# Kernel optimization log

Measured on AMD Instinct MI355X. Metric: run time of the kernel, lower is better.

## Reference

```python
import jax, jax.numpy as jnp
import numpy as np

# ---- Clifford algebra Cl(3,0): 8 blades ordered by grade: [1, e1,e2,e3, e12,e13,e23, e123] ----
_ORDER = [0, 1, 2, 4, 3, 5, 6, 7]  # bitmask of each blade in grade-sorted order
GRADES = np.array([0, 1, 1, 1, 2, 2, 2, 3])  # grade (subspace) of each blade
EPS = 1e-6

def _build_cayley():
    C = np.zeros((8, 8, 8), np.float32)
    for ia, a in enumerate(_ORDER):
        for ib, b in enumerate(_ORDER):
            # reordering sign from anticommuting basis vectors (Euclidean metric -> squares +1)
            t, tot = a >> 1, 0
            while t:
                tot += bin(t & b).count("1")
                t >>= 1
            s = 1.0 if tot % 2 == 0 else -1.0
            C[ia, ib, _ORDER.index(a ^ b)] = s
    return jnp.asarray(C)

CAYLEY = _build_cayley()  # [8,8,8], highly sparse (64 nonzeros)

def mvlinear(x, W, b):
    # x: [B,N,Cin,8], W: [Cout,Cin,4] per-grade weights, b: [Cout] bias on scalar blade
    Wf = W[:, :, GRADES]                               # [Cout,Cin,8] via repeat over grades [1,3,3,1]
    y = jnp.einsum("bnci,oci->bnoi", x, Wf)
    return y.at[..., 0].add(b)

def setup_inputs() -> dict:
    key = jax.random.key(0)
    ks = jax.random.split(key, 5)
    B, N, Cin, Ch = 8, 4096, 64, 128
    return {
        "x": jax.random.normal(ks[0], (B, N, Cin, 8), jnp.float32),
        "W1": jax.random.normal(ks[1], (Ch, Cin, 4), jnp.float32) / np.sqrt(Cin),
        "b1": jax.random.normal(ks[2], (Ch,), jnp.float32) * 0.02,
        "W2": jax.random.normal(ks[3], (Cin, Ch, 4), jnp.float32) / np.sqrt(Ch),
        "b2": jax.random.normal(ks[4], (Cin,), jnp.float32) * 0.02,
        "a": jnp.ones((Cin,), jnp.float32),
    }

def reference(x, W1, b1, W2, b2, a):
    h = mvlinear(x, W1, b1)                                   # [B,N,Ch,8]
    h = jnp.einsum("bnci,ijk,bncj->bnck", h, CAYLEY, h)       # geometric product (sparse Cayley)
    y = mvlinear(h, W2, b2)                                   # [B,N,Cin,8]
    # MVLayerNorm: per-channel multivector norm (Euclidean: sqrt(sum of squares)),
    # averaged over channels, then scale by learned a
    norm = jnp.sqrt(jnp.sum(y * y, axis=-1, keepdims=True))   # [B,N,Cin,1]
    denom = jnp.mean(norm, axis=-2, keepdims=True) + EPS      # [B,N,1,1]
    return a[None, None, :, None] * y / denom
```

## Files before the change

### kernel.cpp

```cpp
#include <hip/hip_runtime.h>
#include <stdint.h>

typedef unsigned short u16;
typedef __attribute__((ext_vector_type(4))) float f32x4;
typedef __attribute__((ext_vector_type(8))) __bf16 bf16x8;

struct Cay { int idx[8][8]; float sgn[8][8]; };
constexpr int kOrder[8] = {0,1,2,4,3,5,6,7};
constexpr int ordpos(int m){ int r=-1; for(int i=0;i<8;i++) if(kOrder[i]==m) r=i; return r; }
constexpr Cay make_cay(){
  Cay c{};
  for(int ia=0; ia<8; ia++) for(int ib=0; ib<8; ib++){
    int a=kOrder[ia], b=kOrder[ib];
    int t=a>>1, tot=0;
    while(t){ int x=t&b; while(x){ tot+=x&1; x>>=1; } t>>=1; }
    c.idx[ia][ib]=ordpos(a^b);
    c.sgn[ia][ib]=(tot&1)?-1.0f:1.0f;
  }
  return c;
}
constexpr Cay CAY = make_cay();

struct GPTab { float dsgn[8]; int np; int pi[28]; int pj[28]; int pk[28]; float ps[28]; };
constexpr GPTab make_gptab(){
  GPTab t{};
  for (int i=0;i<8;i++) t.dsgn[i] = CAY.sgn[i][i];
  t.np = 0;
  for (int i=0;i<8;i++) for (int j=i+1;j<8;j++){
    float s = CAY.sgn[i][j] + CAY.sgn[j][i];
    if (s != 0.0f){ t.pi[t.np]=i; t.pj[t.np]=j; t.pk[t.np]=CAY.idx[i][j];
                    t.ps[t.np]=(s>0.f)?1.0f:-1.0f; t.np++; }
  }
  return t;
}
constexpr GPTab GPT = make_gptab();

__device__ __forceinline__ void gprod_half(const float* h, float* g){
  float g0 = h[0]*h[0];
  #pragma unroll
  for (int i=1;i<8;i++) g0 = fmaf(GPT.dsgn[i]>0.f ? h[i] : -h[i], h[i], g0);
  g[0] = g0;
  #pragma unroll
  for (int k=1;k<8;k++) g[k] = 0.f;
  #pragma unroll
  for (int t=0;t<GPT.np;t++)
    g[GPT.pk[t]] = fmaf(GPT.ps[t]>0.f ? h[GPT.pi[t]] : -h[GPT.pi[t]],
                        h[GPT.pj[t]], g[GPT.pk[t]]);
}

__device__ __forceinline__ u16 f2bf(float f){
  union { float f; uint32_t u; } v; v.f=f;
  uint32_t u=v.u;
  return (u16)((u + 0x7fffu + ((u>>16)&1u)) >> 16);
}

__device__ __forceinline__ uint32_t cvtpk(float lo, float hi){
  uint32_t r;
  asm("v_cvt_pk_bf16_f32 %0, %1, %2" : "=v"(r) : "v"(lo), "v"(hi));
  return r;
}

__global__ void gp_prepack(const float* __restrict__ W1, const float* __restrict__ W2,
                           u16* __restrict__ w1p, u16* __restrict__ w2p)
{
  int t = blockIdx.x*256 + threadIdx.x;
  int e = t & 7, l = (t>>3)&63, f = t>>9;
  int lm = l & 15, lh = l >> 4;
  if (f < 64) {
    int g = f >> 4, ks = (f>>3)&1, ot = f&7;
    int o = ot*16 + lm, c = ks*32 + lh*8 + e;
    w1p[f*512 + l*8 + e] = f2bf(W1[(o*64 + c)*4 + g]);
  } else {
    int f2 = f - 64;
    int g = f2 >> 4, ks = (f2>>2)&3, ot = f2&3;
    int outc = ot*16 + lm, o = ks*32 + lh*8 + e;
    float sc = (g == 0) ? 1.0f : 2.0f;
    w2p[f2*512 + l*8 + e] = f2bf(W2[(outc*128 + o)*4 + g] * sc);
  }
}

__global__ __launch_bounds__(256,4) void gp_fused(
    const float* __restrict__ x, const u16* __restrict__ w1p,
    const float* __restrict__ b1, const u16* __restrict__ w2p,
    const float* __restrict__ b2, const float* __restrict__ avec,
    float* __restrict__ out)
{
  __shared__ __align__(16) char SH[33024];
  float* redArr = reinterpret_cast<float*>(SH + 32768);
  char* G0 = SH + 16384;

  const int tid = threadIdx.x;
  const int w  = tid >> 6;
  const int l  = tid & 63;
  const int lm = l & 15;
  const int lh = l >> 4;
  const int xk = (lm & 7) << 4;

  constexpr int BSTART[4] = {0,1,4,7};
  constexpr int BCNT[4]   = {1,3,3,1};

  const float4* xb  = reinterpret_cast<const float4*>(x);
  const uint4*  w1f = reinterpret_cast<const uint4*>(w1p);
  const uint4*  w2f = reinterpret_cast<const uint4*>(w2p);
  const float4* b1f = reinterpret_cast<const float4*>(b1);

  const int oc = w*16 + lm;
  const float b2v  = b2[oc];
  const float aval = avec[oc];

  {
    const int cp = tid & 31;
    const int pr = tid >> 5;
    const float4* xt = xb + (size_t)blockIdx.x * 2048;
    #pragma unroll
    for (int it=0; it<2; ++it){
      const int p = pr + it*8;
      const float4* src = xt + p*128 + cp*4;
      float4 v0 = src[0], v1 = src[1], v2 = src[2], v3 = src[3];
      uint32_t pk[8];
      pk[0]=cvtpk(v0.x,v2.x); pk[1]=cvtpk(v0.y,v2.y); pk[2]=cvtpk(v0.z,v2.z); pk[3]=cvtpk(v0.w,v2.w);
      pk[4]=cvtpk(v1.x,v3.x); pk[5]=cvtpk(v1.y,v3.y); pk[6]=cvtpk(v1.z,v3.z); pk[7]=cvtpk(v1.w,v3.w);
      const int xo = (p & 7) << 4;
      #pragma unroll
      for (int b=0;b<8;b++)
        *reinterpret_cast<uint32_t*>(SH + (((p*8+b)<<7) + ((cp<<2) ^ xo))) = pk[b];
    }
  }
  __syncthreads();

  {
    f32x4 acc1[8];
    #pragma unroll
    for (int b=0;b<8;++b) acc1[b] = (f32x4){0.f,0.f,0.f,0.f};
    #pragma unroll
    for (int g4=0; g4<4; ++g4){
      #pragma unroll
      for (int ks=0; ks<2; ++ks){
        uint4 wu = w1f[((g4*2+ks)*8 + w)*64 + l];
        bf16x8 wv = __builtin_bit_cast(bf16x8, wu);
        #pragma unroll
        for (int bi=0; bi<3; ++bi){
          if (bi >= BCNT[g4]) break;
          const int blade = BSTART[g4] + bi;
          bf16x8 xv = *reinterpret_cast<const bf16x8*>(
              SH + (((lm*8+blade)<<7) + (((ks*32+lh*8)<<1) ^ xk)));
          acc1[blade] = __builtin_amdgcn_mfma_f32_16x16x32_bf16(wv, xv, acc1[blade], 0,0,0);
        }
      }
    }
    const float4 b14 = b1f[w*4 + lh];
    const float bb[4] = {b14.x, b14.y, b14.z, b14.w};
    uint32_t glo[8], ghi[8];
    #pragma unroll
    for (int rp=0; rp<2; ++rp){
      float ga[8], gb[8];
      { float h[8];
        #pragma unroll
        for (int b=0;b<8;b++) h[b] = acc1[b][rp*2+0];
        h[0] += bb[rp*2+0]; gprod_half(h, ga); }
      { float h[8];
        #pragma unroll
        for (int b=0;b<8;b++) h[b] = acc1[b][rp*2+1];
        h[0] += bb[rp*2+1]; gprod_half(h, gb); }
      #pragma unroll
      for (int b=0;b<8;b++){
        uint32_t v = cvtpk(ga[b], gb[b]);
        if (rp==0) glo[b] = v; else ghi[b] = v;
      }
    }
    const int chB = w*32 + lh*8;
    #pragma unroll
    for (int b=0;b<8;b++){
      uint2 v; v.x = glo[b]; v.y = ghi[b];
      *reinterpret_cast<uint2*>(G0 + (((lm*8+b)<<7) + (chB ^ xk))) = v;
    }
  }
  __syncthreads();

  uint32_t g1lo[8], g1hi[8];
  {
    f32x4 acc1[8];
    #pragma unroll
    for (int b=0;b<8;++b) acc1[b] = (f32x4){0.f,0.f,0.f,0.f};
    #pragma unroll
    for (int g4=0; g4<4; ++g4){
      #pragma unroll
      for (int ks=0; ks<2; ++ks){
        uint4 wu = w1f[((g4*2+ks)*8 + w + 4)*64 + l];
        bf16x8 wv = __builtin_bit_cast(bf16x8, wu);
        #pragma unroll
        for (int bi=0; bi<3; ++bi){
          if (bi >= BCNT[g4]) break;
          const int blade = BSTART[g4] + bi;
          bf16x8 xv = *reinterpret_cast<const bf16x8*>(
              SH + (((lm*8+blade)<<7) + (((ks*32+lh*8)<<1) ^ xk)));
          acc1[blade] = __builtin_amdgcn_mfma_f32_16x16x32_bf16(wv, xv, acc1[blade], 0,0,0);
        }
      }
    }
    const float4 b14 = b1f[(w+4)*4 + lh];
    const float bb[4] = {b14.x, b14.y, b14.z, b14.w};
    #pragma unroll
    for (int rp=0; rp<2; ++rp){
      float ga[8], gb[8];
      { float h[8];
        #pragma unroll
        for (int b=0;b<8;b++) h[b] = acc1[b][rp*2+0];
        h[0] += bb[rp*2+0]; gprod_half(h, ga); }
      { float h[8];
        #pragma unroll
        for (int b=0;b<8;b++) h[b] = acc1[b][rp*2+1];
        h[0] += bb[rp*2+1]; gprod_half(h, gb); }
      #pragma unroll
      for (int b=0;b<8;b++){
        uint32_t v = cvtpk(ga[b], gb[b]);
        if (rp==0) g1lo[b] = v; else g1hi[b] = v;
      }
    }
  }

  f32x4 acc2[8];
  #pragma unroll
  for (int b=0;b<8;++b) acc2[b] = (f32x4){0.f,0.f,0.f,0.f};
  #pragma unroll
  for (int ks=0; ks<2; ++ks){
    #pragma unroll
    for (int g4=0; g4<4; ++g4){
      uint4 wu = w2f[((g4*4+ks)*4 + w)*64 + l];
      bf16x8 wv = __builtin_bit_cast(bf16x8, wu);
      #pragma unroll
      for (int bi=0; bi<3; ++bi){
        if (bi >= BCNT[g4]) break;
        const int blade = BSTART[g4] + bi;
        bf16x8 gv = *reinterpret_cast<const bf16x8*>(
            G0 + (((lm*8+blade)<<7) + ((ks*64 + lh*16) ^ xk)));
        acc2[blade] = __builtin_amdgcn_mfma_f32_16x16x32_bf16(gv, wv, acc2[blade], 0,0,0);
      }
    }
  }
  __syncthreads();

  {
    const int chB = w*32 + lh*8;
    #pragma unroll
    for (int b=0;b<8;b++){
      uint2 v; v.x = g1lo[b]; v.y = g1hi[b];
      *reinterpret_cast<uint2*>(SH + (((lm*8+b)<<7) + (chB ^ xk))) = v;
    }
  }
  __syncthreads();

  #pragma unroll
  for (int ks=2; ks<4; ++ks){
    #pragma unroll
    for (int g4=0; g4<4; ++g4){
      uint4 wu = w2f[((g4*4+ks)*4 + w)*64 + l];
      bf16x8 wv = __builtin_bit_cast(bf16x8, wu);
      #pragma unroll
      for (int bi=0; bi<3; ++bi){
        if (bi >= BCNT[g4]) break;
        const int blade = BSTART[g4] + bi;
        bf16x8 gv = *reinterpret_cast<const bf16x8*>(
            SH + (((lm*8+blade)<<7) + (((ks-2)*64 + lh*16) ^ xk)));
        acc2[blade] = __builtin_amdgcn_mfma_f32_16x16x32_bf16(gv, wv, acc2[blade], 0,0,0);
      }
    }
  }

  #pragma unroll
  for (int r=0; r<4; ++r) acc2[0][r] += b2v;

  float nrm[4];
  #pragma unroll
  for (int r=0; r<4; ++r) {
    float s = 0.f;
    #pragma unroll
    for (int b=0; b<8; ++b) s = fmaf(acc2[b][r], acc2[b][r], s);
    nrm[r] = sqrtf(s);
  }
  #pragma unroll
  for (int r=0; r<4; ++r) {
    float v = nrm[r];
    v += __shfl_xor(v, 1, 64);
    v += __shfl_xor(v, 2, 64);
    v += __shfl_xor(v, 4, 64);
    v += __shfl_xor(v, 8, 64);
    nrm[r] = v;
  }
  if (lm == 0) {
    #pragma unroll
    for (int r=0; r<4; ++r) redArr[(lh*4 + r)*4 + w] = nrm[r];
  }
  __syncthreads();

  #pragma unroll
  for (int r=0; r<4; ++r) {
    const int pos = lh*4 + r;
    const float4 rr = *reinterpret_cast<const float4*>(redArr + pos*4);
    const float denom = (rr.x+rr.y+rr.z+rr.w) * (1.0f/64.0f) + 1e-6f;
    const float sc = aval * __builtin_amdgcn_rcpf(denom);
    float4 o0, o1;
    o0.x = acc2[0][r]*sc; o0.y = acc2[1][r]*sc; o0.z = acc2[2][r]*sc; o0.w = acc2[3][r]*sc;
    o1.x = acc2[4][r]*sc; o1.y = acc2[5][r]*sc; o1.z = acc2[6][r]*sc; o1.w = acc2[7][r]*sc;
    size_t P = (size_t)blockIdx.x*16 + pos;
    float4* op = reinterpret_cast<float4*>(out + (P*64 + (size_t)oc)*8);
    op[0] = o0; op[1] = o1;
  }
}

extern "C" void kernel_launch(void* const* d_in, const int* in_sizes, int n_in,
                              void* d_out, int out_size, void* d_ws, size_t ws_size,
                              hipStream_t stream)
{
  const float* x  = (const float*)d_in[0];
  const float* W1 = (const float*)d_in[1];
  const float* b1 = (const float*)d_in[2];
  const float* W2 = (const float*)d_in[3];
  const float* b2 = (const float*)d_in[4];
  const float* a  = (const float*)d_in[5];
  float* out = (float*)d_out;

  u16* w1p = (u16*)d_ws;
  u16* w2p = w1p + 32768;

  gp_prepack<<<256, 256, 0, stream>>>(W1, W2, w1p, w2p);
  gp_fused<<<2048, 256, 0, stream>>>(x, w1p, b1, w2p, b2, a, out);
}
```

Measured before the change: 44.96 us.

## Loop each block over four tiles with register-held W1 and prefetched x

The fused kernel becomes a persistent-style loop: each block handles four 16-point tiles, so the grid shrinks to 512 blocks and launch bounds drop to 2 blocks per CU. W1 fragments and the biases are loaded once into registers before the loop instead of per tile. The next tile's x is prefetched with inline-asm global loads and manual vmcnt waits, so its fetch overlaps the current tile's MFMA work. The aim is to hide global-memory latency and amortise the weight loads, at the cost of higher register pressure, lower occupancy and fragile hand-written waitcnt logic that the compiler cannot check.

```diff
diff --git a/kernel.cpp b/kernel.cpp
--- a/kernel.cpp
+++ b/kernel.cpp
@@ -3,6 +3,7 @@
 
 typedef unsigned short u16;
 typedef __attribute__((ext_vector_type(4))) float f32x4;
+typedef __attribute__((ext_vector_type(4))) unsigned int u32x4;
 typedef __attribute__((ext_vector_type(8))) __bf16 bf16x8;
 
 struct Cay { int idx[8][8]; float sgn[8][8]; };
@@ -79,7 +80,20 @@
   }
 }
 
-__global__ __launch_bounds__(256,4) void gp_fused(
+#define PF_ISSUE(TILE) do {                                                   \
+    const float4* _a0 = xb + (size_t)(TILE)*2048 + pr*128 + cp*4;             \
+    const float4* _a1 = _a0 + 1024;                                           \
+    asm volatile("global_load_dwordx4 %0, %1, off"           : "=v"(rx[0]) : "v"(_a0) : "memory"); \
+    asm volatile("global_load_dwordx4 %0, %1, off offset:16" : "=v"(rx[1]) : "v"(_a0) : "memory"); \
+    asm volatile("global_load_dwordx4 %0, %1, off offset:32" : "=v"(rx[2]) : "v"(_a0) : "memory"); \
+    asm volatile("global_load_dwordx4 %0, %1, off offset:48" : "=v"(rx[3]) : "v"(_a0) : "memory"); \
+    asm volatile("global_load_dwordx4 %0, %1, off"           : "=v"(rx[4]) : "v"(_a1) : "memory"); \
+    asm volatile("global_load_dwordx4 %0, %1, off offset:16" : "=v"(rx[5]) : "v"(_a1) : "memory"); \
+    asm volatile("global_load_dwordx4 %0, %1, off offset:32" : "=v"(rx[6]) : "v"(_a1) : "memory"); \
+    asm volatile("global_load_dwordx4 %0, %1, off offset:48" : "=v"(rx[7]) : "v"(_a1) : "memory"); \
+  } while(0)
+
+__global__ __launch_bounds__(256,2) void gp_fused(
     const float* __restrict__ x, const u16* __restrict__ w1p,
     const float* __restrict__ b1, const u16* __restrict__ w2p,
     const float* __restrict__ b2, const float* __restrict__ avec,
@@ -95,216 +109,184 @@
   const int lm = l & 15;
   const int lh = l >> 4;
   const int xk = (lm & 7) << 4;
+  const int cp = tid & 31;
+  const int pr = tid >> 5;
 
   constexpr int BSTART[4] = {0,1,4,7};
   constexpr int BCNT[4]   = {1,3,3,1};
 
   const float4* xb  = reinterpret_cast<const float4*>(x);
-  const uint4*  w1f = reinterpret_cast<const uint4*>(w1p);
   const uint4*  w2f = reinterpret_cast<const uint4*>(w2p);
-  const float4* b1f = reinterpret_cast<const float4*>(b1);
-
   const int oc = w*16 + lm;
-  const float b2v  = b2[oc];
-  const float aval = avec[oc];
-
-  {
-    const int cp = tid & 31;
-    const int pr = tid >> 5;
-    const float4* xt = xb + (size_t)blockIdx.x * 2048;
+
+  u32x4 w1r[16];
+  #pragma unroll
+  for (int i=0; i<8; ++i){
+    const u16* a0 = w1p + (size_t)((i*8 + w    )*64 + l)*8;
+    const u16* a1 = w1p + (size_t)((i*8 + w + 4)*64 + l)*8;
+    asm volatile("global_load_dwordx4 %0, %1, off" : "=v"(w1r[i*2+0]) : "v"(a0) : "memory");
+    asm volatile("global_load_dwordx4 %0, %1, off" : "=v"(w1r[i*2+1]) : "v"(a1) : "memory");
+  }
+  f32x4 b1v0, b1v1;
+  float b2v, aval;
+  asm volatile("global_load_dwordx4 %0, %1, off" : "=v"(b1v0) : "v"(b1 + (size_t)(w*4+lh)*4)     : "memory");
+  asm volatile("global_load_dwordx4 %0, %1, off" : "=v"(b1v1) : "v"(b1 + (size_t)((w+4)*4+lh)*4) : "memory");
+  asm volatile("global_load_dword %0, %1, off"   : "=v"(b2v)  : "v"(b2 + oc)   : "memory");
+  asm volatile("global_load_dword %0, %1, off"   : "=v"(aval) : "v"(avec + oc) : "memory");
+
+  f32x4 rx[8];
+  PF_ISSUE((size_t)blockIdx.x*4);
+  asm volatile("s_waitcnt vmcnt(0)" ::: "memory");
+  __builtin_amdgcn_sched_barrier(0);
+
+  #pragma unroll 1
+  for (int t=0; t<4; ++t){
+    const size_t tile = (size_t)blockIdx.x*4 + t;
+
+    asm volatile("s_waitcnt vmcnt(8)" ::: "memory");
+    __builtin_amdgcn_sched_barrier(0);
+
     #pragma unroll
     for (int it=0; it<2; ++it){
       const int p = pr + it*8;
-      const float4* src = xt + p*128 + cp*4;
-      float4 v0 = src[0], v1 = src[1], v2 = src[2], v3 = src[3];
+      f32x4 v0=rx[it*4+0], v1=rx[it*4+1], v2=rx[it*4+2], v3=rx[it*4+3];
       uint32_t pk[8];
-      pk[0]=cvtpk(v0.x,v2.x); pk[1]=cvtpk(v0.y,v2.y); pk[2]=cvtpk(v0.z,v2.z); pk[3]=cvtpk(v0.w,v2.w);
-      pk[4]=cvtpk(v1.x,v3.x); pk[5]=cvtpk(v1.y,v3.y); pk[6]=cvtpk(v1.z,v3.z); pk[7]=cvtpk(v1.w,v3.w);
+      pk[0]=cvtpk(v0[0],v2[0]); pk[1]=cvtpk(v0[1],v2[1]); pk[2]=cvtpk(v0[2],v2[2]); pk[3]=cvtpk(v0[3],v2[3]);
+      pk[4]=cvtpk(v1[0],v3[0]); pk[5]=cvtpk(v1[1],v3[1]); pk[6]=cvtpk(v1[2],v3[2]); pk[7]=cvtpk(v1[3],v3[3]);
       const int xo = (p & 7) << 4;
       #pragma unroll
       for (int b=0;b<8;b++)
         *reinterpret_cast<uint32_t*>(SH + (((p*8+b)<<7) + ((cp<<2) ^ xo))) = pk[b];
     }
-  }
-  __syncthreads();
-
-  {
-    f32x4 acc1[8];
-    #pragma unroll
-    for (int b=0;b<8;++b) acc1[b] = (f32x4){0.f,0.f,0.f,0.f};
-    #pragma unroll
-    for (int g4=0; g4<4; ++g4){
-      #pragma unroll
-      for (int ks=0; ks<2; ++ks){
-        uint4 wu = w1f[((g4*2+ks)*8 + w)*64 + l];
+    __syncthreads();
+
+    if (t < 3) PF_ISSUE(tile + 1);
+
+    uint32_t g1lo[8], g1hi[8];
+    #pragma unroll
+    for (int cc=0; cc<2; ++cc){
+      f32x4 acc1[8];
+      #pragma unroll
+      for (int b=0;b<8;++b) acc1[b] = (f32x4){0.f,0.f,0.f,0.f};
+      #pragma unroll
+      for (int g4=0; g4<4; ++g4){
+        #pragma unroll
+        for (int ks=0; ks<2; ++ks){
+          bf16x8 wv = __builtin_bit_cast(bf16x8, w1r[(g4*2+ks)*2 + cc]);
+          #pragma unroll
+          for (int bi=0; bi<3; ++bi){
+            if (bi >= BCNT[g4]) break;
+            const int blade = BSTART[g4] + bi;
+            bf16x8 xv = *reinterpret_cast<const bf16x8*>(
+                SH + (((lm*8+blade)<<7) + (((ks*32+lh*8)<<1) ^ xk)));
+            acc1[blade] = __builtin_amdgcn_mfma_f32_16x16x32_bf16(wv, xv, acc1[blade], 0,0,0);
+          }
+        }
+      }
+      const f32x4 b14 = cc ? b1v1 : b1v0;
+      const float bb[4] = {b14[0], b14[1], b14[2], b14[3]};
+      uint32_t glo[8], ghi[8];
+      #pragma unroll
+      for (int rp=0; rp<2; ++rp){
+        float ga[8], gb[8];
+        { float h[8];
+          #pragma unroll
+          for (int b=0;b<8;b++) h[b] = acc1[b][rp*2+0];
+          h[0] += bb[rp*2+0]; gprod_half(h, ga); }
+        { float h[8];
+          #pragma unroll
+          for (int b=0;b<8;b++) h[b] = acc1[b][rp*2+1];
+          h[0] += bb[rp*2+1]; gprod_half(h, gb); }
+        #pragma unroll
+        for (int b=0;b<8;b++){
+          uint32_t v = cvtpk(ga[b], gb[b]);
+          if (rp==0) glo[b] = v; else ghi[b] = v;
+        }
+      }
+      if (cc == 0){
+        const int chB = w*32 + lh*8;
+        #pragma unroll
+        for (int b=0;b<8;b++){
+          uint2 v; v.x = glo[b]; v.y = ghi[b];
+          *reinterpret_cast<uint2*>(G0 + (((lm*8+b)<<7) + (chB ^ xk))) = v;
+        }
+      } else {
+        #pragma unroll
+        for (int b=0;b<8;b++){ g1lo[b] = glo[b]; g1hi[b] = ghi[b]; }
+      }
+    }
+    __syncthreads();
+
+    {
+      const int chB = w*32 + lh*8;
+      #pragma unroll
+      for (int b=0;b<8;b++){
+        uint2 v; v.x = g1lo[b]; v.y = g1hi[b];
+        *reinterpret_cast<uint2*>(SH + (((lm*8+b)<<7) + (chB ^ xk))) = v;
+      }
+    }
+    __syncthreads();
+
+    f32x4 acc2[8];
+    #pragma unroll
+    for (int b=0;b<8;++b) acc2[b] = (f32x4){0.f,0.f,0.f,0.f};
+    #pragma unroll
+    for (int ks=0; ks<4; ++ks){
+      #pragma unroll
+      for (int g4=0; g4<4; ++g4){
+        uint4 wu = w2f[((g4*4+ks)*4 + w)*64 + l];
         bf16x8 wv = __builtin_bit_cast(bf16x8, wu);
         #pragma unroll
         for (int bi=0; bi<3; ++bi){
           if (bi >= BCNT[g4]) break;
           const int blade = BSTART[g4] + bi;
-          bf16x8 xv = *reinterpret_cast<const bf16x8*>(
-              SH + (((lm*8+blade)<<7) + (((ks*32+lh*8)<<1) ^ xk)));
-          acc1[blade] = __builtin_amdgcn_mfma_f32_16x16x32_bf16(wv, xv, acc1[blade], 0,0,0);
+          const char* gp = (ks < 2)
+              ? (G0 + (((lm*8+blade)<<7) + ((ks*64 + lh*16) ^ xk)))
+              : (SH + (((lm*8+blade)<<7) + (((ks-2)*64 + lh*16) ^ xk)));
+          bf16x8 gv = *reinterpret_cast<const bf16x8*>(gp);
+          acc2[blade] = __builtin_amdgcn_mfma_f32_16x16x32_bf16(gv, wv, acc2[blade], 0,0,0);
         }
       }
     }
-    const float4 b14 = b1f[w*4 + lh];
-    const float bb[4] = {b14.x, b14.y, b14.z, b14.w};
-    uint32_t glo[8], ghi[8];
-    #pragma unroll
-    for (int rp=0; rp<2; ++rp){
-      float ga[8], gb[8];
-      { float h[8];
-        #pragma unroll
-        for (int b=0;b<8;b++) h[b] = acc1[b][rp*2+0];
-        h[0] += bb[rp*2+0]; gprod_half(h, ga); }
-      { float h[8];
-        #pragma unroll
-        for (int b=0;b<8;b++) h[b] = acc1[b][rp*2+1];
-        h[0] += bb[rp*2+1]; gprod_half(h, gb); }
-      #pragma unroll
-      for (int b=0;b<8;b++){
-        uint32_t v = cvtpk(ga[b], gb[b]);
-        if (rp==0) glo[b] = v; else ghi[b] = v;
-      }
-    }
-    const int chB = w*32 + lh*8;
-    #pragma unroll
-    for (int b=0;b<8;b++){
-      uint2 v; v.x = glo[b]; v.y = ghi[b];
-      *reinterpret_cast<uint2*>(G0 + (((lm*8+b)<<7) + (chB ^ xk))) = v;
-    }
-  }
-  __syncthreads();
-
-  uint32_t g1lo[8], g1hi[8];
-  {
-    f32x4 acc1[8];
-    #pragma unroll
-    for (int b=0;b<8;++b) acc1[b] = (f32x4){0.f,0.f,0.f,0.f};
-    #pragma unroll
-    for (int g4=0; g4<4; ++g4){
-      #pragma unroll
-      for (int ks=0; ks<2; ++ks){
-        uint4 wu = w1f[((g4*2+ks)*8 + w + 4)*64 + l];
-        bf16x8 wv = __builtin_bit_cast(bf16x8, wu);
-        #pragma unroll
-        for (int bi=0; bi<3; ++bi){
-          if (bi >= BCNT[g4]) break;
-          const int blade = BSTART[g4] + bi;
-          bf16x8 xv = *reinterpret_cast<const bf16x8*>(
-              SH + (((lm*8+blade)<<7) + (((ks*32+lh*8)<<1) ^ xk)));
-          acc1[blade] = __builtin_amdgcn_mfma_f32_16x16x32_bf16(wv, xv, acc1[blade], 0,0,0);
-        }
-      }
-    }
-    const float4 b14 = b1f[(w+4)*4 + lh];
-    const float bb[4] = {b14.x, b14.y, b14.z, b14.w};
-    #pragma unroll
-    for (int rp=0; rp<2; ++rp){
-      float ga[8], gb[8];
-      { float h[8];
-        #pragma unroll
-        for (int b=0;b<8;b++) h[b] = acc1[b][rp*2+0];
-        h[0] += bb[rp*2+0]; gprod_half(h, ga); }
-      { float h[8];
-        #pragma unroll
-        for (int b=0;b<8;b++) h[b] = acc1[b][rp*2+1];
-        h[0] += bb[rp*2+1]; gprod_half(h, gb); }
-      #pragma unroll
-      for (int b=0;b<8;b++){
-        uint32_t v = cvtpk(ga[b], gb[b]);
-        if (rp==0) g1lo[b] = v; else g1hi[b] = v;
-      }
-    }
-  }
-
-  f32x4 acc2[8];
-  #pragma unroll
-  for (int b=0;b<8;++b) acc2[b] = (f32x4){0.f,0.f,0.f,0.f};
-  #pragma unroll
-  for (int ks=0; ks<2; ++ks){
-    #pragma unroll
-    for (int g4=0; g4<4; ++g4){
-      uint4 wu = w2f[((g4*4+ks)*4 + w)*64 + l];
-      bf16x8 wv = __builtin_bit_cast(bf16x8, wu);
-      #pragma unroll
-      for (int bi=0; bi<3; ++bi){
-        if (bi >= BCNT[g4]) break;
-        const int blade = BSTART[g4] + bi;
-        bf16x8 gv = *reinterpret_cast<const bf16x8*>(
-            G0 + (((lm*8+blade)<<7) + ((ks*64 + lh*16) ^ xk)));
-        acc2[blade] = __builtin_amdgcn_mfma_f32_16x16x32_bf16(gv, wv, acc2[blade], 0,0,0);
-      }
-    }
-  }
-  __syncthreads();
-
-  {
-    const int chB = w*32 + lh*8;
-    #pragma unroll
-    for (int b=0;b<8;b++){
-      uint2 v; v.x = g1lo[b]; v.y = g1hi[b];
-      *reinterpret_cast<uint2*>(SH + (((lm*8+b)<<7) + (chB ^ xk))) = v;
-    }
-  }
-  __syncthreads();
-
-  #pragma unroll
-  for (int ks=2; ks<4; ++ks){
-    #pragma unroll
-    for (int g4=0; g4<4; ++g4){
-      uint4 wu = w2f[((g4*4+ks)*4 + w)*64 + l];
-      bf16x8 wv = __builtin_bit_cast(bf16x8, wu);
-      #pragma unroll
-      for (int bi=0; bi<3; ++bi){
-        if (bi >= BCNT[g4]) break;
-        const int blade = BSTART[g4] + bi;
-        bf16x8 gv = *reinterpret_cast<const bf16x8*>(
-            SH + (((lm*8+blade)<<7) + (((ks-2)*64 + lh*16) ^ xk)));
-        acc2[blade] = __builtin_amdgcn_mfma_f32_16x16x32_bf16(gv, wv, acc2[blade], 0,0,0);
-      }
-    }
-  }
-
-  #pragma unroll
-  for (int r=0; r<4; ++r) acc2[0][r] += b2v;
-
-  float nrm[4];
-  #pragma unroll
-  for (int r=0; r<4; ++r) {
-    float s = 0.f;
-    #pragma unroll
-    for (int b=0; b<8; ++b) s = fmaf(acc2[b][r], acc2[b][r], s);
-    nrm[r] = sqrtf(s);
-  }
-  #pragma unroll
-  for (int r=0; r<4; ++r) {
-    float v = nrm[r];
-    v += __shfl_xor(v, 1, 64);
-    v += __shfl_xor(v, 2, 64);
-    v += __shfl_xor(v, 4, 64);
-    v += __shfl_xor(v, 8, 64);
-    nrm[r] = v;
-  }
-  if (lm == 0) {
-    #pragma unroll
-    for (int r=0; r<4; ++r) redArr[(lh*4 + r)*4 + w] = nrm[r];
-  }
-  __syncthreads();
-
-  #pragma unroll
-  for (int r=0; r<4; ++r) {
-    const int pos = lh*4 + r;
-    const float4 rr = *reinterpret_cast<const float4*>(redArr + pos*4);
-    const float denom = (rr.x+rr.y+rr.z+rr.w) * (1.0f/64.0f) + 1e-6f;
-    const float sc = aval * __builtin_amdgcn_rcpf(denom);
-    float4 o0, o1;
-    o0.x = acc2[0][r]*sc; o0.y = acc2[1][r]*sc; o0.z = acc2[2][r]*sc; o0.w = acc2[3][r]*sc;
-    o1.x = acc2[4][r]*sc; o1.y = acc2[5][r]*sc; o1.z = acc2[6][r]*sc; o1.w = acc2[7][r]*sc;
-    size_t P = (size_t)blockIdx.x*16 + pos;
-    float4* op = reinterpret_cast<float4*>(out + (P*64 + (size_t)oc)*8);
-    op[0] = o0; op[1] = o1;
+
+    #pragma unroll
+    for (int r=0; r<4; ++r) acc2[0][r] += b2v;
+    float nrm[4];
+    #pragma unroll
+    for (int r=0; r<4; ++r){
+      float s = 0.f;
+      #pragma unroll
+      for (int b=0; b<8; ++b) s = fmaf(acc2[b][r], acc2[b][r], s);
+      nrm[r] = sqrtf(s);
+    }
+    #pragma unroll
+    for (int r=0; r<4; ++r){
+      float v = nrm[r];
+      v += __shfl_xor(v, 1, 64);
+      v += __shfl_xor(v, 2, 64);
+      v += __shfl_xor(v, 4, 64);
+      v += __shfl_xor(v, 8, 64);
+      nrm[r] = v;
+    }
+    if (lm == 0){
+      #pragma unroll
+      for (int r=0; r<4; ++r) redArr[(lh*4 + r)*4 + w] = nrm[r];
+    }
+    __syncthreads();
+
+    #pragma unroll
+    for (int r=0; r<4; ++r){
+      const int pos = lh*4 + r;
+      const float4 rr = *reinterpret_cast<const float4*>(redArr + pos*4);
+      const float denom = (rr.x+rr.y+rr.z+rr.w) * (1.0f/64.0f) + 1e-6f;
+      const float sc = aval * __builtin_amdgcn_rcpf(denom);
+      float4 o0, o1;
+      o0.x = acc2[0][r]*sc; o0.y = acc2[1][r]*sc; o0.z = acc2[2][r]*sc; o0.w = acc2[3][r]*sc;
+      o1.x = acc2[4][r]*sc; o1.y = acc2[5][r]*sc; o1.z = acc2[6][r]*sc; o1.w = acc2[7][r]*sc;
+      size_t P = tile*16 + pos;
+      float4* op = reinterpret_cast<float4*>(out + (P*64 + (size_t)oc)*8);
+      op[0] = o0; op[1] = o1;
+    }
   }
 }
 
@@ -324,5 +306,5 @@
   u16* w2p = w1p + 32768;
 
   gp_prepack<<<256, 256, 0, stream>>>(W1, W2, w1p, w2p);
-  gp_fused<<<2048, 256, 0, stream>>>(x, w1p, b1, w2p, b2, a, out);
-}
+  gp_fused<<<512, 256, 0, stream>>>(x, w1p, b1, w2p, b2, a, out);
+}
```

Result: slower. 47.86 us (+6.5%).
